# Performance work log

Measured on AMD Instinct MI355X. Metric: run time of the kernel, lower is better.

Reference implementation:

```python
import jax, jax.numpy as jnp
import numpy as np

B, S, E, D, H, L = 128, 50, 512, 1024, 16, 4
V, NU, NF, NR = 100000, 50000, 10000, 5
DK = D // H
FF = 4 * D


def _pe(S, D):
    # FranchisePositionalEncoding: two interleaved sin/cos halves (chrono + release*1.5)
    half = D // 2
    pos = jnp.arange(S, dtype=jnp.float32)[:, None]
    div = jnp.exp(jnp.arange(0, half, 2, dtype=jnp.float32) * (-np.log(10000.0) / half))
    def il(a):
        return jnp.stack([jnp.sin(a), jnp.cos(a)], axis=-1).reshape(S, half)
    return jnp.concatenate([il(pos * div), il(pos * div * 1.5)], axis=-1)  # [S, D]


def _ln(x, g, b):
    m = x.mean(-1, keepdims=True)
    v = ((x - m) ** 2).mean(-1, keepdims=True)
    return (x - m) * jax.lax.rsqrt(v + 1e-5) * g + b


def _gelu(x):
    return jax.nn.gelu(x, approximate=False)


def setup_inputs() -> dict:
    key = jax.random.key(0)
    ks = iter(jax.random.split(key, 64))
    def p(shape, s=0.02):
        return jax.random.normal(next(ks), shape, jnp.float32) * s
    inp = {
        'movie_table': p((V, E)), 'fran_table': p((NF, E)), 'entry_table': p((NR, E)),
        'proj_w': p((3 * E, D)), 'proj_b': jnp.zeros((D,), jnp.float32),
        'wq': p((L, D, D)), 'bq': jnp.zeros((L, D), jnp.float32),
        'wk': p((L, D, D)), 'bk': jnp.zeros((L, D), jnp.float32),
        'wv': p((L, D, D)), 'bv': jnp.zeros((L, D), jnp.float32),
        'wo': p((L, D, D)), 'bo': jnp.zeros((L, D), jnp.float32),
        'rel_table': p((L, NR, DK)),
        'aln_g': jnp.ones((L, D), jnp.float32), 'aln_b': jnp.zeros((L, D), jnp.float32),
        'f_w1': p((L, D, FF)), 'f_b1': jnp.zeros((L, FF), jnp.float32),
        'f_w2': p((L, FF, D)), 'f_b2': jnp.zeros((L, D), jnp.float32),
        'ln_g': jnp.ones((L, D), jnp.float32), 'ln_b': jnp.zeros((L, D), jnp.float32),
        'user_table': p((NU, D)),
        'mq_w': p((D, D)), 'mq_b': jnp.zeros((D,), jnp.float32),
        'mk_w': p((D, D)), 'mk_b': jnp.zeros((D,), jnp.float32),
        'mv_w': p((D, D)), 'mv_b': jnp.zeros((D,), jnp.float32),
        'mo_w': p((D, D)), 'mo_b': jnp.zeros((D,), jnp.float32),
        'c_w1': p((2 * D, D)), 'c_b1': jnp.zeros((D,), jnp.float32),
        'c_w2': p((D, 1)), 'c_b2': jnp.zeros((1,), jnp.float32),
        'n_w1': p((2 * D, D)), 'n_b1': jnp.zeros((D,), jnp.float32),
        'n_w2': p((D, V)), 'n_b2': jnp.zeros((V,), jnp.float32),
        'r_w1': p((3 * D, D)), 'r_b1': jnp.zeros((D,), jnp.float32),
        'r_w2': p((D, 1)), 'r_b2': jnp.zeros((1,), jnp.float32),
        'o_w1': p((D, D // 2)), 'o_b1': jnp.zeros((D // 2,), jnp.float32),
        'o_w2': p((D // 2, 2)), 'o_b2': jnp.zeros((2,), jnp.float32),
        'user_ids': jax.random.randint(next(ks), (B,), 0, NU),
        'movie_ids': jax.random.randint(next(ks), (B, S), 0, V),
        'franchise_ids': jax.random.randint(next(ks), (B, S), 0, NF),
        'entry_types': jax.random.randint(next(ks), (B, S), 0, NR),
        'relation_matrix': jax.random.randint(next(ks), (S, S), 0, NR),
    }
    return inp


def reference(movie_table, fran_table, entry_table, proj_w, proj_b,
              wq, bq, wk, bk, wv, bv, wo, bo, rel_table, aln_g, aln_b,
              f_w1, f_b1, f_w2, f_b2, ln_g, ln_b, user_table,
              mq_w, mq_b, mk_w, mk_b, mv_w, mv_b, mo_w, mo_b,
              c_w1, c_b1, c_w2, c_b2, n_w1, n_b1, n_w2, n_b2,
              r_w1, r_b1, r_w2, r_b2, o_w1, o_b1, o_w2, o_b2,
              user_ids, movie_ids, franchise_ids, entry_types, relation_matrix):
    b, s = movie_ids.shape
    d = proj_w.shape[1]
    nl, _, dk = rel_table.shape
    h = d // dk
    scale = 1.0 / np.sqrt(dk).astype(np.float32)

    # encoder input: concat(movie, franchise, entry) embeddings -> proj -> +PE
    x = jnp.concatenate([movie_table[movie_ids], fran_table[franchise_ids],
                         entry_table[entry_types]], axis=-1) @ proj_w + proj_b
    x = x + _pe(s, d)

    for l in range(nl):
        res = x
        q = (x @ wq[l] + bq[l]).reshape(b, s, h, dk).transpose(0, 2, 1, 3)  # [b,h,s,dk]
        k = (x @ wk[l] + bk[l]).reshape(b, s, h, dk).transpose(0, 2, 1, 3)
        v = (x @ wv[l] + bv[l]).reshape(b, s, h, dk).transpose(0, 2, 1, 3)
        scores = jnp.einsum('bhid,bhjd->bhij', q, k) * scale
        rel = rel_table[l][relation_matrix]  # [s,s,dk]
        scores = scores + 0.5 * jnp.einsum('bhid,ijd->bhij', q, rel)
        attn = jax.nn.softmax(scores, axis=-1)
        ctx = jnp.einsum('bhij,bhjd->bhid', attn, v).transpose(0, 2, 1, 3).reshape(b, s, d)
        x = _ln(ctx @ wo[l] + bo[l] + res, aln_g[l], aln_b[l])
        ff = _gelu(x @ f_w1[l] + f_b1[l]) @ f_w2[l] + f_b2[l]
        x = _ln(x + ff, ln_g[l], ln_b[l])

    # user preference cross-attention (nn.MultiheadAttention, q_len=1)
    user_emb = user_table[user_ids]  # [b,d]
    qh = (user_emb @ mq_w + mq_b).reshape(b, h, dk)
    kh = (x @ mk_w + mk_b).reshape(b, s, h, dk)
    vh = (x @ mv_w + mv_b).reshape(b, s, h, dk)
    a = jax.nn.softmax(jnp.einsum('bhd,bshd->bhs', qh, kh) * scale, axis=-1)
    user_pref = jnp.einsum('bhs,bshd->bhd', a, vh).reshape(b, d) @ mo_w + mo_b

    seq_repr = x.mean(axis=1)  # mask is None path
    ci = jnp.concatenate([user_pref, seq_repr], axis=-1)
    completion = jax.nn.sigmoid(_gelu(ci @ c_w1 + c_b1) @ c_w2 + c_b2)
    next_logits = _gelu(ci @ n_w1 + n_b1) @ n_w2 + n_b2
    ri = jnp.concatenate([user_emb, user_pref, seq_repr], axis=-1)
    rating = _gelu(ri @ r_w1 + r_b1) @ r_w2 + r_b2
    order = jax.nn.softmax(_gelu(user_pref @ o_w1 + o_b1) @ o_w2 + o_b2, axis=-1)
    return (x, completion, next_logits, rating, order, user_pref)
```

## Files before the change

### kernel.cpp

```cpp
#include <hip/hip_runtime.h>
#include <hip/hip_bf16.h>
#include <math.h>

#define B_   128
#define S_   50
#define BS_  (B_*S_)
#define E_   512
#define D_   1024
#define H_   16
#define DK_  64
#define L_   4
#define FF_  4096
#define V_   100000

typedef short bf8_t __attribute__((ext_vector_type(8)));
typedef float f32x4 __attribute__((ext_vector_type(4)));
typedef float f32x16 __attribute__((ext_vector_type(16)));
typedef unsigned short u16;

__device__ __forceinline__ float gelu_exact(float x) {
    return 0.5f * x * (1.0f + erff(x * 0.70710678118654752440f));
}
__device__ __forceinline__ u16 f2bf(float f) {
    unsigned int u = __float_as_uint(f);
    return (u16)((u + 0x7FFFu + ((u >> 16) & 1u)) >> 16);
}
__device__ __forceinline__ float bf2f(u16 u) {
    return __uint_as_float(((unsigned int)u) << 16);
}

__device__ __forceinline__ void gload16(const u16* g, u16* l) {
    auto* g1 = reinterpret_cast<const __attribute__((address_space(1))) unsigned int*>(
                   reinterpret_cast<uintptr_t>(g));
    auto* l3 = reinterpret_cast<__attribute__((address_space(3))) unsigned int*>(
                   reinterpret_cast<uintptr_t>(l));
    __builtin_amdgcn_global_load_lds(g1, l3, 16, 0, 0);
}

__device__ __forceinline__ void wtrans_body(
    const float* __restrict__ W, u16* __restrict__ Wt,
    int K, int N, int nb, int kb, int dstRowOff)
{
    __shared__ float t[32][33];
    int c = threadIdx.x & 31, r0 = threadIdx.x >> 5;
    #pragma unroll
    for (int rr = 0; rr < 32; rr += 8)
        t[rr + r0][c] = W[(size_t)(kb + rr + r0) * N + nb + c];
    __syncthreads();
    #pragma unroll
    for (int rr = 0; rr < 32; rr += 8)
        Wt[(size_t)(dstRowOff + nb + rr + r0) * K + kb + c] = f2bf(t[c][rr + r0]);
}

__global__ __launch_bounds__(256) void wtrans(
    const float* __restrict__ W, u16* __restrict__ Wt,
    int K, int N, long srcLS, long dstLS, int dstRowOff)
{
    int l = blockIdx.z;
    wtrans_body(W + (size_t)l * srcLS, Wt + (size_t)l * dstLS,
                K, N, blockIdx.x * 32, blockIdx.y * 32, dstRowOff);
}

__global__ __launch_bounds__(256) void wtrans_qkv(
    const float* __restrict__ wq, const float* __restrict__ wk, const float* __restrict__ wv,
    u16* __restrict__ dst)
{
    int z = blockIdx.z;
    int l = z & 3, which = z >> 2;
    const float* W = (which == 0 ? wq : which == 1 ? wk : wv) + (size_t)l * (D_ * D_);
    u16* Wt = dst + (size_t)l * (3 * D_ * D_) + (size_t)which * (D_ * D_);
    wtrans_body(W, Wt, D_, D_, blockIdx.x * 32, blockIdx.y * 32, 0);
}

struct WT8 { const float* s[8]; u16* d[8]; };
__global__ __launch_bounds__(256) void wtrans8(WT8 p)
{
    int z = blockIdx.z;
    wtrans_body(p.s[z], p.d[z], D_, D_, blockIdx.x * 32, blockIdx.y * 32, 0);
}

__global__ __launch_bounds__(256) void wtrans_ff(
    const float* __restrict__ w1, const float* __restrict__ w2,
    u16* __restrict__ d1, u16* __restrict__ d2)
{
    if (blockIdx.z == 0)
        wtrans_body(w1, d1, D_, FF_, blockIdx.x * 32, blockIdx.y * 32, 0);
    else
        wtrans_body(w2, d2, FF_, D_, blockIdx.y * 32, blockIdx.x * 32, 0);
}

__global__ __launch_bounds__(256) void embed_concat(
    const float* __restrict__ mt, const float* __restrict__ ft, const float* __restrict__ et,
    const int* __restrict__ mids, const int* __restrict__ fids, const int* __restrict__ eids,
    u16* __restrict__ xinb)
{
    int bs = blockIdx.x;
    int mid = mids[bs], fid = fids[bs], eid = eids[bs];
    const float* srcs[3] = { mt + (size_t)mid * E_, ft + (size_t)fid * E_, et + (size_t)eid * E_ };
    u16* dst = xinb + (size_t)bs * (3 * E_);
    for (int i = threadIdx.x; i < 384; i += 256) {
        int seg = i >> 7, off = i & 127;
        float4 v = reinterpret_cast<const float4*>(srcs[seg])[off];
        ushort4 b;
        b.x = f2bf(v.x); b.y = f2bf(v.y); b.z = f2bf(v.z); b.w = f2bf(v.w);
        reinterpret_cast<ushort4*>(dst + seg * E_)[off] = b;
    }
}

__global__ __launch_bounds__(256) void setup_misc(
    const float* __restrict__ bq, const float* __restrict__ bk, const float* __restrict__ bv,
    const float* __restrict__ cb1, const float* __restrict__ nb1,
    const float* __restrict__ mkb, const float* __restrict__ mvb,
    float* __restrict__ bqkv, float* __restrict__ bcn, float* __restrict__ bkv,
    float* __restrict__ pet)
{
    int bi = blockIdx.x, tid = threadIdx.x;
    if (bi < 4) {
        for (int c = tid; c < 3072; c += 256) {
            float v = (c < 1024) ? bq[bi * 1024 + c]
                    : (c < 2048) ? bk[bi * 1024 + c - 1024]
                                 : bv[bi * 1024 + c - 2048];
            bqkv[bi * 3072 + c] = v;
        }
    } else if (bi == 4) {
        for (int c = tid; c < 2048; c += 256)
            bcn[c] = (c < 1024) ? cb1[c] : nb1[c - 1024];
    } else if (bi == 5) {
        for (int c = tid; c < 2048; c += 256)
            bkv[c] = (c < 1024) ? mkb[c] : mvb[c - 1024];
    } else {
        int s = bi - 6;
        const float cc = -logf(10000.0f) / 512.0f;
        for (int d = tid; d < D_; d += 256) {
            int second = d >= 512;
            int c2 = second ? d - 512 : d;
            int i = c2 >> 1;
            float div = expf(cc * (float)(2 * i));
            float aa = (float)s * div * (second ? 1.5f : 1.0f);
            pet[s * D_ + d] = (c2 & 1) ? cosf(aa) : sinf(aa);
        }
    }
}

__global__ __launch_bounds__(256) void gemm128_w32(
    const u16* __restrict__ A, int lda, const u16* __restrict__ Wt,
    const float* __restrict__ bias,
    u16* __restrict__ Cb, int ldcb,
    int N, int K, int act)
{
    __shared__ u16 As[2 * 4096];
    __shared__ u16 Bs[2 * 4096];
    const int tid  = threadIdx.x;
    const int lane = tid & 63;
    const int wid  = tid >> 6;
    const int wr   = wid >> 1, wc = wid & 1;

    const int gx  = gridDim.x;
    const int nwg = gx * gridDim.y;
    int orig = blockIdx.y * gx + blockIdx.x;
    int qq = nwg >> 3, rr2 = nwg & 7, xcd = orig & 7, idx = orig >> 3;
    int wgid = (xcd < rr2) ? (xcd * (qq + 1) + idx)
                           : (rr2 * (qq + 1) + (xcd - rr2) * qq + idx);
    const int rowBase = (wgid / gx) * 128;
    const int colBase = (wgid % gx) * 128;

    const int sRowL  = lane >> 2;
    const int sChunk = lane & 3;
    const int gRow0  = (wid << 5) + sRowL;
    const int skey   = (gRow0 >> 1) & 3;
    const int gC     = (sChunk ^ skey) << 3;
    const u16* aS0 = A  + (size_t)(rowBase + gRow0) * lda + gC;
    const u16* aS1 = aS0 + (size_t)16 * lda;
    const u16* bS0 = Wt + (size_t)(colBase + gRow0) * K + gC;
    const u16* bS1 = bS0 + (size_t)16 * K;
    const int ldsW0 = (wid << 5) << 5;
    const int ldsW1 = ldsW0 + (16 << 5);

    const int l31 = lane & 31;
    const int hi5 = lane >> 5;
    const int key32 = (l31 >> 1) & 3;
    const int c0 = (0 | hi5) ^ key32;
    const int c1 = (2 | hi5) ^ key32;
    const int aB0 = (wr * 64 + l31) * 32;
    const int bB0 = (wc * 64 + l31) * 32;

    f32x16 acc[2][2] = {};
    const int nk = K >> 5;

    auto STAGE = [&](int kb, int buf) {
        u16* dA = As + buf * 4096;
        u16* dB = Bs + buf * 4096;
        gload16(aS0 + kb, dA + ldsW0);
        gload16(aS1 + kb, dA + ldsW1);
        gload16(bS0 + kb, dB + ldsW0);
        gload16(bS1 + kb, dB + ldsW1);
    };

    STAGE(0, 0);
    __builtin_amdgcn_sched_barrier(0);
    STAGE(32, 1);
    __builtin_amdgcn_sched_barrier(0);
    asm volatile("s_waitcnt vmcnt(4)\n\ts_barrier" ::: "memory");
    __builtin_amdgcn_sched_barrier(0);

    for (int t = 0; t < nk; ++t) {
        const int cur = t & 1;
        const u16* bA = As + cur * 4096;
        const u16* bB = Bs + cur * 4096;
        bf8_t aF[2][2], bF[2][2];
        #pragma unroll
        for (int mi = 0; mi < 2; ++mi) {
            aF[mi][0] = *reinterpret_cast<const bf8_t*>(&bA[aB0 + mi * 1024 + c0 * 8]);
            aF[mi][1] = *reinterpret_cast<const bf8_t*>(&bA[aB0 + mi * 1024 + c1 * 8]);
        }
        #pragma unroll
        for (int ni = 0; ni < 2; ++ni) {
            bF[ni][0] = *reinterpret_cast<const bf8_t*>(&bB[bB0 + ni * 1024 + c0 * 8]);
            bF[ni][1] = *reinterpret_cast<const bf8_t*>(&bB[bB0 + ni * 1024 + c1 * 8]);
        }
        #pragma unroll
        for (int mi = 0; mi < 2; ++mi)
            #pragma unroll
            for (int ni = 0; ni < 2; ++ni) {
                acc[mi][ni] = __builtin_amdgcn_mfma_f32_32x32x16_bf16(aF[mi][0], bF[ni][0], acc[mi][ni], 0, 0, 0);
                acc[mi][ni] = __builtin_amdgcn_mfma_f32_32x32x16_bf16(aF[mi][1], bF[ni][1], acc[mi][ni], 0, 0, 0);
            }
        if (t == nk - 1) break;
        __builtin_amdgcn_sched_barrier(0);
        asm volatile("s_waitcnt lgkmcnt(0)\n\ts_barrier" ::: "memory");
        __builtin_amdgcn_sched_barrier(0);
        if (t + 2 < nk) {
            STAGE((t + 2) << 5, cur);
            __builtin_amdgcn_sched_barrier(0);
            asm volatile("s_waitcnt vmcnt(4)\n\ts_barrier" ::: "memory");
        } else {
            asm volatile("s_waitcnt vmcnt(0)\n\ts_barrier" ::: "memory");
        }
        __builtin_amdgcn_sched_barrier(0);
    }

    #pragma unroll
    for (int mi = 0; mi < 2; ++mi) {
        int rt = rowBase + wr * 64 + mi * 32 + 4 * hi5;
        #pragma unroll
        for (int ni = 0; ni < 2; ++ni) {
            int ct = colBase + wc * 64 + ni * 32 + l31;
            float bv = bias ? bias[ct] : 0.0f;
            #pragma unroll
            for (int r = 0; r < 16; ++r) {
                int rr = rt + (r & 3) + 8 * (r >> 2);
                float v = acc[mi][ni][r] + bv;
                if (act == 1) v = gelu_exact(v);
                Cb[(size_t)rr * ldcb + ct] = f2bf(v);
            }
        }
    }
}

__global__ __launch_bounds__(256) void gemm_sk32(
    const u16* __restrict__ A, int lda, const u16* __restrict__ Wt, int ldb,
    u16* __restrict__ P0, u16* __restrict__ P1,
    int N, int Kh)
{
    __shared__ u16 As[2 * 4096];
    __shared__ u16 Bs[2 * 4096];
    const int tid  = threadIdx.x;
    const int lane = tid & 63;
    const int wid  = tid >> 6;
    const int wr   = wid >> 1, wc = wid & 1;

    const int gx  = gridDim.x;
    const int nwg = gx * gridDim.y;
    int orig = blockIdx.y * gx + blockIdx.x;
    int qq = nwg >> 3, rr2 = nwg & 7, xcd = orig & 7, idx = orig >> 3;
    int wgid = (xcd < rr2) ? (xcd * (qq + 1) + idx)
                           : (rr2 * (qq + 1) + (xcd - rr2) * qq + idx);
    const int rowBase = (wgid / gx) * 128;
    const int colBase = (wgid % gx) * 128;
    const int k0 = blockIdx.z * Kh;
    u16* P = blockIdx.z ? P1 : P0;

    const int sRowL  = lane >> 2;
    const int sChunk = lane & 3;
    const int gRow0  = (wid << 5) + sRowL;
    const int skey   = (gRow0 >> 1) & 3;
    const int gC     = (sChunk ^ skey) << 3;
    const u16* aS0 = A  + (size_t)(rowBase + gRow0) * lda + k0 + gC;
    const u16* aS1 = aS0 + (size_t)16 * lda;
    const u16* bS0 = Wt + (size_t)(colBase + gRow0) * ldb + k0 + gC;
    const u16* bS1 = bS0 + (size_t)16 * ldb;
    const int ldsW0 = (wid << 5) << 5;
    const int ldsW1 = ldsW0 + (16 << 5);

    const int l31 = lane & 31;
    const int hi5 = lane >> 5;
    const int key32 = (l31 >> 1) & 3;
    const int c0 = (0 | hi5) ^ key32;
    const int c1 = (2 | hi5) ^ key32;
    const int aB0 = (wr * 64 + l31) * 32;
    const int bB0 = (wc * 64 + l31) * 32;

    f32x16 acc[2][2] = {};
    const int nk = Kh >> 5;

    auto STAGE = [&](int kb, int buf) {
        u16* dA = As + buf * 4096;
        u16* dB = Bs + buf * 4096;
        gload16(aS0 + kb, dA + ldsW0);
        gload16(aS1 + kb, dA + ldsW1);
        gload16(bS0 + kb, dB + ldsW0);
        gload16(bS1 + kb, dB + ldsW1);
    };

    STAGE(0, 0);
    __builtin_amdgcn_sched_barrier(0);
    STAGE(32, 1);
    __builtin_amdgcn_sched_barrier(0);
    asm volatile("s_waitcnt vmcnt(4)\n\ts_barrier" ::: "memory");
    __builtin_amdgcn_sched_barrier(0);

    for (int t = 0; t < nk; ++t) {
        const int cur = t & 1;
        const u16* bA = As + cur * 4096;
        const u16* bB = Bs + cur * 4096;
        bf8_t aF[2][2], bF[2][2];
        #pragma unroll
        for (int mi = 0; mi < 2; ++mi) {
            aF[mi][0] = *reinterpret_cast<const bf8_t*>(&bA[aB0 + mi * 1024 + c0 * 8]);
            aF[mi][1] = *reinterpret_cast<const bf8_t*>(&bA[aB0 + mi * 1024 + c1 * 8]);
        }
        #pragma unroll
        for (int ni = 0; ni < 2; ++ni) {
            bF[ni][0] = *reinterpret_cast<const bf8_t*>(&bB[bB0 + ni * 1024 + c0 * 8]);
            bF[ni][1] = *reinterpret_cast<const bf8_t*>(&bB[bB0 + ni * 1024 + c1 * 8]);
        }
        #pragma unroll
        for (int mi = 0; mi < 2; ++mi)
            #pragma unroll
            for (int ni = 0; ni < 2; ++ni) {
                acc[mi][ni] = __builtin_amdgcn_mfma_f32_32x32x16_bf16(aF[mi][0], bF[ni][0], acc[mi][ni], 0, 0, 0);
                acc[mi][ni] = __builtin_amdgcn_mfma_f32_32x32x16_bf16(aF[mi][1], bF[ni][1], acc[mi][ni], 0, 0, 0);
            }
        if (t == nk - 1) break;
        __builtin_amdgcn_sched_barrier(0);
        asm volatile("s_waitcnt lgkmcnt(0)\n\ts_barrier" ::: "memory");
        __builtin_amdgcn_sched_barrier(0);
        if (t + 2 < nk) {
            STAGE((t + 2) << 5, cur);
            __builtin_amdgcn_sched_barrier(0);
            asm volatile("s_waitcnt vmcnt(4)\n\ts_barrier" ::: "memory");
        } else {
            asm volatile("s_waitcnt vmcnt(0)\n\ts_barrier" ::: "memory");
        }
        __builtin_amdgcn_sched_barrier(0);
    }

    #pragma unroll
    for (int mi = 0; mi < 2; ++mi) {
        int rt = rowBase + wr * 64 + mi * 32 + 4 * hi5;
        #pragma unroll
        for (int ni = 0; ni < 2; ++ni) {
            int ct = colBase + wc * 64 + ni * 32 + l31;
            #pragma unroll
            for (int r = 0; r < 16; ++r) {
                int rr = rt + (r & 3) + 8 * (r >> 2);
                P[(size_t)rr * N + ct] = f2bf(acc[mi][ni][r]);
            }
        }
    }
}

__global__ __launch_bounds__(256) void combine_bias_pe(
    const u16* __restrict__ p1, const u16* __restrict__ p2,
    const float* __restrict__ bias, const float* __restrict__ pe,
    u16* __restrict__ outb)
{
    int row = blockIdx.x, tid = threadIdx.x;
    int c0 = tid << 2;
    size_t base = (size_t)row * D_ + c0;
    ushort4 v1 = *reinterpret_cast<const ushort4*>(p1 + base);
    ushort4 v2 = *reinterpret_cast<const ushort4*>(p2 + base);
    float4 bv = *reinterpret_cast<const float4*>(bias + c0);
    float4 pv = *reinterpret_cast<const float4*>(pe + (size_t)(row % S_) * D_ + c0);
    ushort4 ob;
    ob.x = f2bf(bf2f(v1.x) + bf2f(v2.x) + bv.x + pv.x);
    ob.y = f2bf(bf2f(v1.y) + bf2f(v2.y) + bv.y + pv.y);
    ob.z = f2bf(bf2f(v1.z) + bf2f(v2.z) + bv.z + pv.z);
    ob.w = f2bf(bf2f(v1.w) + bf2f(v2.w) + bv.w + pv.w);
    *reinterpret_cast<ushort4*>(outb + base) = ob;
}

__global__ __launch_bounds__(256) void add_ln2(
    const u16* __restrict__ p1, const u16* __restrict__ p2,
    const float* __restrict__ bias, const u16* __restrict__ res,
    const float* __restrict__ g, const float* __restrict__ be,
    u16* __restrict__ outb, float* __restrict__ outf)
{
    int row = blockIdx.x, tid = threadIdx.x;
    int c0 = tid << 2;
    size_t base = (size_t)row * D_ + c0;
    ushort4 v1 = *reinterpret_cast<const ushort4*>(p1 + base);
    ushort4 v2 = *reinterpret_cast<const ushort4*>(p2 + base);
    float4 bv = *reinterpret_cast<const float4*>(bias + c0);
    ushort4 vr = *reinterpret_cast<const ushort4*>(res + base);
    float vals[4] = { bf2f(v1.x) + bf2f(v2.x) + bv.x + bf2f(vr.x),
                      bf2f(v1.y) + bf2f(v2.y) + bv.y + bf2f(vr.y),
                      bf2f(v1.z) + bf2f(v2.z) + bv.z + bf2f(vr.z),
                      bf2f(v1.w) + bf2f(v2.w) + bv.w + bf2f(vr.w) };
    float s = vals[0] + vals[1] + vals[2] + vals[3];
    __shared__ float red[8];
    #pragma unroll
    for (int off = 32; off; off >>= 1) s += __shfl_xor(s, off);
    int wave = tid >> 6, lane = tid & 63;
    if (lane == 0) red[wave] = s;
    __syncthreads();
    float mean = (red[0] + red[1] + red[2] + red[3]) * (1.0f / D_);
    float vv = 0.0f;
    #pragma unroll
    for (int t = 0; t < 4; ++t) {
        float d = vals[t] - mean;
        vv += d * d;
    }
    #pragma unroll
    for (int off = 32; off; off >>= 1) vv += __shfl_xor(vv, off);
    if (lane == 0) red[4 + wave] = vv;
    __syncthreads();
    float var = (red[4] + red[5] + red[6] + red[7]) * (1.0f / D_);
    float rstd = rsqrtf(var + 1e-5f);
    float4 gv  = *reinterpret_cast<const float4*>(g  + c0);
    float4 bev = *reinterpret_cast<const float4*>(be + c0);
    float o0 = (vals[0] - mean) * rstd * gv.x + bev.x;
    float o1 = (vals[1] - mean) * rstd * gv.y + bev.y;
    float o2 = (vals[2] - mean) * rstd * gv.z + bev.z;
    float o3 = (vals[3] - mean) * rstd * gv.w + bev.w;
    ushort4 ob;
    ob.x = f2bf(o0); ob.y = f2bf(o1); ob.z = f2bf(o2); ob.w = f2bf(o3);
    *reinterpret_cast<ushort4*>(outb + base) = ob;
    if (outf) {
        float4 of = { o0, o1, o2, o3 };
        *reinterpret_cast<float4*>(outf + base) = of;
    }
}

template<int BM>
__global__ __launch_bounds__(256) void gemm_bf16_t(
    const u16* __restrict__ A, int lda, const u16* __restrict__ Wt,
    const float* __restrict__ bias, float* __restrict__ Cf,
    u16* __restrict__ Cb, int ldcb, u16* __restrict__ Cb2, int ldcb2,
    int N, int K, int act)
{
    constexpr int MR   = BM / 32;
    constexpr int AL   = BM / 64;
    constexpr int ABUF = BM * 32;
    __shared__ u16 As[2 * ABUF];
    __shared__ u16 Bs[2 * 4096];
    const int tid  = threadIdx.x;
    const int lane = tid & 63;
    const int wid  = tid >> 6;
    const int wr   = wid >> 1, wc = wid & 1;

    const int rowBase = blockIdx.y * BM;
    const int colBase = blockIdx.x * 128;

    const int fr = lane & 15;
    const int hi = lane >> 4;

    const int sRowL  = lane >> 2;
    const int sChunk = lane & 3;
    const int aRow0 = wid * (BM / 4) + sRowL;
    const int aKey  = (aRow0 >> 1) & 3;
    const u16* aS0 = A + (size_t)(rowBase + aRow0) * lda + ((sChunk ^ aKey) << 3);
    const u16* aS1 = aS0 + (size_t)16 * lda;
    const int ldsA0 = (wid * (BM / 4)) * 32;
    const int ldsA1 = ldsA0 + 512;
    const int bRow0 = wid * 32 + sRowL;
    const int bKey  = (bRow0 >> 1) & 3;
    const u16* bS0 = Wt + (size_t)(colBase + bRow0) * K + ((sChunk ^ bKey) << 3);
    const u16* bS1 = bS0 + (size_t)16 * K;
    const int ldsB0 = (wid * 32) * 32;
    const int ldsB1 = ldsB0 + 512;

    const int swz = ((hi ^ ((fr >> 1) & 3)) << 3);
    const int aRd = (wr * (BM / 2) + fr) * 32 + swz;
    const int bRd = (wc * 64 + fr) * 32 + swz;

    f32x4 acc[MR][4] = {};
    const int nk = K >> 5;

    auto STAGE = [&](int kb, int buf) {
        u16* dA = As + buf * ABUF;
        u16* dB = Bs + buf * 4096;
        gload16(aS0 + kb, dA + ldsA0);
        if constexpr (AL == 2) gload16(aS1 + kb, dA + ldsA1);
        gload16(bS0 + kb, dB + ldsB0);
        gload16(bS1 + kb, dB + ldsB1);
    };

    STAGE(0, 0);
    __builtin_amdgcn_sched_barrier(0);
    STAGE(32, 1);
    __builtin_amdgcn_sched_barrier(0);
    if constexpr (BM == 128) asm volatile("s_waitcnt vmcnt(4)\n\ts_barrier" ::: "memory");
    else                     asm volatile("s_waitcnt vmcnt(3)\n\ts_barrier" ::: "memory");
    __builtin_amdgcn_sched_barrier(0);

    for (int t = 0; t < nk; ++t) {
        const int cur = t & 1;
        const u16* bA = As + cur * ABUF;
        const u16* bB = Bs + cur * 4096;
        bf8_t af[MR], bf[4];
        #pragma unroll
        for (int m = 0; m < MR; ++m)
            af[m] = *reinterpret_cast<const bf8_t*>(&bA[aRd + m * 512]);
        #pragma unroll
        for (int n = 0; n < 4; ++n)
            bf[n] = *reinterpret_cast<const bf8_t*>(&bB[bRd + n * 512]);
        #pragma unroll
        for (int m = 0; m < MR; ++m)
            #pragma unroll
            for (int n = 0; n < 4; ++n)
                acc[m][n] = __builtin_amdgcn_mfma_f32_16x16x32_bf16(af[m], bf[n], acc[m][n], 0, 0, 0);
        if (t == nk - 1) break;
        __builtin_amdgcn_sched_barrier(0);
        asm volatile("s_waitcnt lgkmcnt(0)\n\ts_barrier" ::: "memory");
        __builtin_amdgcn_sched_barrier(0);
        if (t + 2 < nk) {
            STAGE((t + 2) << 5, cur);
            __builtin_amdgcn_sched_barrier(0);
            if constexpr (BM == 128) asm volatile("s_waitcnt vmcnt(4)\n\ts_barrier" ::: "memory");
            else                     asm volatile("s_waitcnt vmcnt(3)\n\ts_barrier" ::: "memory");
        } else {
            asm volatile("s_waitcnt vmcnt(0)\n\ts_barrier" ::: "memory");
        }
        __builtin_amdgcn_sched_barrier(0);
    }

    const int orow = hi << 2;
    #pragma unroll
    for (int m = 0; m < MR; ++m) {
        int r0 = rowBase + wr * (BM / 2) + m * 16 + orow;
        #pragma unroll
        for (int n = 0; n < 4; ++n) {
            int c = colBase + wc * 64 + n * 16 + fr;
            float bv = bias ? bias[c] : 0.0f;
            #pragma unroll
            for (int r = 0; r < 4; ++r) {
                float v = acc[m][n][r] + bv;
                if (act == 1) v = gelu_exact(v);
                if (Cf)  Cf [(size_t)(r0 + r) * N + c] = v;
                if (Cb)  Cb [(size_t)(r0 + r) * ldcb  + c] = f2bf(v);
                if (Cb2) Cb2[(size_t)(r0 + r) * ldcb2 + c] = f2bf(v);
            }
        }
    }
}

__global__ __launch_bounds__(256) void gemm_logits(
    const float* __restrict__ A, int lda, const float* __restrict__ W,
    const float* __restrict__ bias, float* __restrict__ C, int N, int K)
{
    __shared__ u16 As[2][128][40];
    __shared__ u16 Bs[2][128][40];
    const int tid  = threadIdx.x;
    const int lane = tid & 63;
    const int wid  = tid >> 6;
    const int wr   = wid >> 1, wc = wid & 1;
    const int colBase = blockIdx.x * 128;

    const int a_r = tid >> 1;
    const int a_h = (tid & 1) << 4;
    const int b_c = tid & 127;
    const int b_h = (tid >> 7) << 4;

    const int fr = lane & 15;
    const int fk = (lane >> 4) << 3;

    f32x4 acc[4][4] = {};
    const int nvalid = N - colBase;
    const bool valid = b_c < nvalid;
    const int nk = K >> 5;

    float4 aR[4];
    float  bR[16];

    auto LD = [&](int kb) {
        const float* Ap = A + (size_t)a_r * lda + kb + a_h;
        #pragma unroll
        for (int q = 0; q < 4; ++q)
            aR[q] = *reinterpret_cast<const float4*>(Ap + q * 4);
        const float* Wp = W + (size_t)(kb + b_h) * N + colBase + b_c;
        #pragma unroll
        for (int kk = 0; kk < 16; ++kk)
            bR[kk] = valid ? Wp[(size_t)kk * N] : 0.0f;
    };
    auto ST = [&](int buf) {
        #pragma unroll
        for (int q = 0; q < 4; ++q) {
            ushort4 bb;
            bb.x = f2bf(aR[q].x); bb.y = f2bf(aR[q].y);
            bb.z = f2bf(aR[q].z); bb.w = f2bf(aR[q].w);
            *reinterpret_cast<ushort4*>(&As[buf][a_r][a_h + q * 4]) = bb;
        }
        u16 tmp[16];
        #pragma unroll
        for (int kk = 0; kk < 16; ++kk) tmp[kk] = f2bf(bR[kk]);
        *reinterpret_cast<bf8_t*>(&Bs[buf][b_c][b_h])     = *reinterpret_cast<const bf8_t*>(tmp);
        *reinterpret_cast<bf8_t*>(&Bs[buf][b_c][b_h + 8]) = *reinterpret_cast<const bf8_t*>(tmp + 8);
    };

    LD(0); ST(0);
    __syncthreads();

    for (int t = 0; t < nk; ++t) {
        if (t + 1 < nk) LD((t + 1) << 5);
        const int cur = t & 1;
        bf8_t af[4], bfv[4];
        #pragma unroll
        for (int m = 0; m < 4; ++m)
            af[m] = *reinterpret_cast<const bf8_t*>(&As[cur][wr * 64 + m * 16 + fr][fk]);
        #pragma unroll
        for (int n = 0; n < 4; ++n)
            bfv[n] = *reinterpret_cast<const bf8_t*>(&Bs[cur][wc * 64 + n * 16 + fr][fk]);
        #pragma unroll
        for (int m = 0; m < 4; ++m)
            #pragma unroll
            for (int n = 0; n < 4; ++n)
                acc[m][n] = __builtin_amdgcn_mfma_f32_16x16x32_bf16(af[m], bfv[n], acc[m][n], 0, 0, 0);
        if (t + 1 < nk) ST(cur ^ 1);
        __syncthreads();
    }

    const int orow = (lane >> 4) << 2;
    #pragma unroll
    for (int m = 0; m < 4; ++m) {
        int r0 = wr * 64 + m * 16 + orow;
        #pragma unroll
        for (int n = 0; n < 4; ++n) {
            int c = colBase + wc * 64 + n * 16 + fr;
            if (c < N) {
                float bv = bias ? bias[c] : 0.0f;
                #pragma unroll
                for (int r = 0; r < 4; ++r)
                    C[(size_t)(r0 + r) * N + c] = acc[m][n][r] + bv;
            }
        }
    }
}

__global__ __launch_bounds__(256) void attn_kernel(
    const u16* __restrict__ qkv, const float* __restrict__ rt, const int* __restrict__ rm,
    u16* __restrict__ ctxb)
{
    int bh = blockIdx.x;
    int b = bh >> 4, h = bh & 15;
    __shared__ float qs[S_][DK_ + 1], ks[S_][DK_ + 1], vs[S_][DK_ + 1];
    __shared__ float rts[5][DK_];
    __shared__ float Rs[S_][8];
    int tid = threadIdx.x;
    int wave = tid >> 6, lane = tid & 63;

    for (int idx = tid; idx < S_ * DK_; idx += 256) {
        int s = idx >> 6, d = idx & 63;
        size_t g = ((size_t)(b * S_ + s)) * (3 * D_) + h * DK_ + d;
        qs[s][d] = bf2f(qkv[g]);
        ks[s][d] = bf2f(qkv[g + D_]);
        vs[s][d] = bf2f(qkv[g + 2 * D_]);
    }
    for (int i = tid; i < 5 * DK_; i += 256)
        rts[i >> 6][i & 63] = rt[i];
    __syncthreads();

    for (int t = tid; t < S_ * 5; t += 256) {
        int i = t / 5, r = t - 5 * i;
        float a = 0.0f;
        #pragma unroll 8
        for (int d = 0; d < DK_; ++d) a += qs[i][d] * rts[r][d];
        Rs[i][r] = a;
    }
    __syncthreads();

    const float scale = 0.125f;
    for (int i = wave; i < S_; i += 4) {
        float sc = -INFINITY;
        if (lane < S_) {
            float acc = 0.0f;
            #pragma unroll 8
            for (int d = 0; d < DK_; ++d) acc += qs[i][d] * ks[lane][d];
            sc = acc * scale + 0.5f * Rs[i][rm[i * S_ + lane]];
        }
        float m = sc;
        #pragma unroll
        for (int off = 32; off; off >>= 1) m = fmaxf(m, __shfl_xor(m, off));
        float e = (lane < S_) ? expf(sc - m) : 0.0f;
        float sum = e;
        #pragma unroll
        for (int off = 32; off; off >>= 1) sum += __shfl_xor(sum, off);
        float aval = e / sum;

        float acc = 0.0f;
        for (int j = 0; j < S_; ++j) {
            float aj = __shfl(aval, j);
            acc += aj * vs[j][lane];
        }
        ctxb[((size_t)(b * S_ + i)) * D_ + h * DK_ + lane] = f2bf(acc);
    }
}

__global__ __launch_bounds__(256) void gather_user(
    const float* __restrict__ ut, const int* __restrict__ ids,
    u16* __restrict__ o1, int ld1, u16* __restrict__ o2, int ld2)
{
    int b = blockIdx.x;
    int uid = ids[b];
    for (int d = threadIdx.x; d < D_; d += 256) {
        u16 v = f2bf(ut[(size_t)uid * D_ + d]);
        o1[(size_t)b * ld1 + d] = v;
        o2[(size_t)b * ld2 + d] = v;
    }
}

__global__ __launch_bounds__(64) void cross_attn(
    const u16* __restrict__ qh, const u16* __restrict__ kv, u16* __restrict__ up)
{
    int bh = blockIdx.x;
    int b = bh >> 4, h = bh & 15;
    int lane = threadIdx.x;
    __shared__ float qv[DK_];
    qv[lane] = bf2f(qh[(size_t)b * D_ + h * DK_ + lane]);
    __syncthreads();
    float sc = -INFINITY;
    if (lane < S_) {
        float acc = 0.0f;
        const u16* krow = kv + ((size_t)(b * S_ + lane)) * 2048 + h * DK_;
        #pragma unroll 8
        for (int d = 0; d < DK_; ++d) acc += qv[d] * bf2f(krow[d]);
        sc = acc * 0.125f;
    }
    float m = sc;
    #pragma unroll
    for (int off = 32; off; off >>= 1) m = fmaxf(m, __shfl_xor(m, off));
    float e = (lane < S_) ? expf(sc - m) : 0.0f;
    float sum = e;
    #pragma unroll
    for (int off = 32; off; off >>= 1) sum += __shfl_xor(sum, off);
    float aval = e / sum;
    float acc = 0.0f;
    for (int j = 0; j < S_; ++j) {
        float aj = __shfl(aval, j);
        acc += aj * bf2f(kv[((size_t)(b * S_ + j)) * 2048 + 1024 + h * DK_ + lane]);
    }
    up[(size_t)b * D_ + h * DK_ + lane] = f2bf(acc);
}

__global__ __launch_bounds__(256) void seq_mean(
    const float* __restrict__ x,
    u16* __restrict__ o1, int ld1, u16* __restrict__ o2, int ld2)
{
    int b = blockIdx.x;
    for (int d = threadIdx.x; d < D_; d += 256) {
        float s = 0.0f;
        for (int si = 0; si < S_; ++si)
            s += x[((size_t)(b * S_ + si)) * D_ + d];
        u16 v = f2bf(s * (1.0f / S_));
        o1[(size_t)b * ld1 + d] = v;
        o2[(size_t)b * ld2 + d] = v;
    }
}

__global__ __launch_bounds__(256) void heads_final(
    const float* __restrict__ h1cn, const float* __restrict__ h1r, const float* __restrict__ ho,
    const float* __restrict__ c_w2, const float* __restrict__ c_b2,
    const float* __restrict__ r_w2, const float* __restrict__ r_b2,
    const float* __restrict__ o_w2, const float* __restrict__ o_b2,
    float* __restrict__ comp, float* __restrict__ rating, float* __restrict__ order)
{
    int b = blockIdx.x;
    int lane = threadIdx.x & 63, wv = threadIdx.x >> 6;
    if (wv == 0) {
        float s = 0.0f;
        for (int d = lane; d < D_; d += 64) s += h1cn[(size_t)b * 2048 + d] * c_w2[d];
        #pragma unroll
        for (int off = 32; off; off >>= 1) s += __shfl_xor(s, off);
        if (lane == 0) comp[b] = 1.0f / (1.0f + expf(-(s + c_b2[0])));
    } else if (wv == 1) {
        float s = 0.0f;
        for (int d = lane; d < D_; d += 64) s += h1r[(size_t)b * D_ + d] * r_w2[d];
        #pragma unroll
        for (int off = 32; off; off >>= 1) s += __shfl_xor(s, off);
        if (lane == 0) rating[b] = s + r_b2[0];
    } else if (wv == 2) {
        float s0 = 0.0f, s1 = 0.0f;
        for (int d = lane; d < 512; d += 64) {
            float hv = ho[(size_t)b * 512 + d];
            s0 += hv * o_w2[d * 2];
            s1 += hv * o_w2[d * 2 + 1];
        }
        #pragma unroll
        for (int off = 32; off; off >>= 1) { s0 += __shfl_xor(s0, off); s1 += __shfl_xor(s1, off); }
        if (lane == 0) {
            float a = s0 + o_b2[0], c = s1 + o_b2[1];
            float m = fmaxf(a, c);
            float ea = expf(a - m), ec = expf(c - m);
            float s = ea + ec;
            order[b * 2] = ea / s;
            order[b * 2 + 1] = ec / s;
        }
    }
}

extern "C" void kernel_launch(void* const* d_in, const int* in_sizes, int n_in,
                              void* d_out, int out_size, void* d_ws, size_t ws_size,
                              hipStream_t stream) {
    const float* movie_table = (const float*)d_in[0];
    const float* fran_table  = (const float*)d_in[1];
    const float* entry_table = (const float*)d_in[2];
    const float* proj_w      = (const float*)d_in[3];
    const float* proj_b      = (const float*)d_in[4];
    const float* wq          = (const float*)d_in[5];
    const float* bq          = (const float*)d_in[6];
    const float* wk          = (const float*)d_in[7];
    const float* bk          = (const float*)d_in[8];
    const float* wv          = (const float*)d_in[9];
    const float* bv          = (const float*)d_in[10];
    const float* wo          = (const float*)d_in[11];
    const float* bo          = (const float*)d_in[12];
    const float* rel_table   = (const float*)d_in[13];
    const float* aln_g       = (const float*)d_in[14];
    const float* aln_b       = (const float*)d_in[15];
    const float* f_w1        = (const float*)d_in[16];
    const float* f_b1        = (const float*)d_in[17];
    const float* f_w2        = (const float*)d_in[18];
    const float* f_b2        = (const float*)d_in[19];
    const float* ln_g        = (const float*)d_in[20];
    const float* ln_b        = (const float*)d_in[21];
    const float* user_table  = (const float*)d_in[22];
    const float* mq_w        = (const float*)d_in[23];
    const float* mq_b        = (const float*)d_in[24];
    const float* mk_w        = (const float*)d_in[25];
    const float* mk_b        = (const float*)d_in[26];
    const float* mv_w        = (const float*)d_in[27];
    const float* mv_b        = (const float*)d_in[28];
    const float* mo_w        = (const float*)d_in[29];
    const float* mo_b        = (const float*)d_in[30];
    const float* c_w1        = (const float*)d_in[31];
    const float* c_b1        = (const float*)d_in[32];
    const float* c_w2        = (const float*)d_in[33];
    const float* c_b2        = (const float*)d_in[34];
    const float* n_w1        = (const float*)d_in[35];
    const float* n_b1        = (const float*)d_in[36];
    const float* n_w2        = (const float*)d_in[37];
    const float* n_b2        = (const float*)d_in[38];
    const float* r_w1        = (const float*)d_in[39];
    const float* r_b1        = (const float*)d_in[40];
    const float* r_w2        = (const float*)d_in[41];
    const float* r_b2        = (const float*)d_in[42];
    const float* o_w1        = (const float*)d_in[43];
    const float* o_b1        = (const float*)d_in[44];
    const float* o_w2        = (const float*)d_in[45];
    const float* o_b2        = (const float*)d_in[46];
    const int* user_ids      = (const int*)d_in[47];
    const int* movie_ids     = (const int*)d_in[48];
    const int* franchise_ids = (const int*)d_in[49];
    const int* entry_types   = (const int*)d_in[50];
    const int* relation_mat  = (const int*)d_in[51];

    u16* up16 = (u16*)d_ws;
    u16* proj_wt = up16;
    u16* wqkv_t  = proj_wt + (size_t)1024 * 1536;
    u16* wo_t    = wqkv_t  + (size_t)4 * 3072 * 1024;
    u16* fw1_buf = wo_t    + (size_t)4 * 1024 * 1024;
    u16* fw2_buf = fw1_buf + (size_t)4096 * 1024;
    u16* mq_t    = fw2_buf + (size_t)1024 * 4096;
    u16* mk_t    = mq_t    + (size_t)1024 * 1024;
    u16* mv_t    = mk_t    + (size_t)1024 * 1024;
    u16* mo_t    = mv_t    + (size_t)1024 * 1024;
    u16* cn_w1t  = mo_t    + (size_t)1024 * 1024;
    u16* r_w1t   = cn_w1t  + (size_t)2048 * 2048;
    u16* o_w1t   = r_w1t   + (size_t)1024 * 3072;
    u16* ffb     = o_w1t   + (size_t)512 * 1024;
    u16* xinb    = ffb;
    u16* xb      = ffb     + (size_t)BS_ * FF_;
    u16* xb2     = xb      + (size_t)BS_ * D_;
    u16* qkvb    = xb2     + (size_t)BS_ * D_;
    u16* kvb     = qkvb    + (size_t)BS_ * 3 * D_;
    u16* ctxb    = kvb;
    u16* ueb     = kvb     + (size_t)BS_ * 2 * D_;
    u16* upb_pre = ueb     + (size_t)B_ * D_;
    u16* cib     = upb_pre + (size_t)B_ * D_;
    u16* rib     = cib     + (size_t)B_ * 2 * D_;
    float* fp    = (float*)(rib + (size_t)B_ * 3 * D_);
    float* bqkv  = fp;
    float* bcn   = bqkv + 4 * 3072;
    float* bkv   = bcn  + 2048;
    float* pet   = bkv  + 2048;
    float* h1cn  = pet  + 50 * 1024;
    float* h1r   = h1cn + (size_t)B_ * 2048;
    float* ho    = h1r  + (size_t)B_ * D_;

    u16* pQK = qkvb;
    u16* pKV = kvb;
    u16* pFF = ffb;

    float* xout    = (float*)d_out;
    float* comp    = xout + (size_t)BS_ * D_;
    float* logits  = comp + B_;
    float* rating  = logits + (size_t)B_ * V_;
    float* order   = rating + B_;
    float* upref   = order + 2 * B_;

    dim3 blk(256);

    wtrans<<<dim3(32, 48, 1), blk, 0, stream>>>(proj_w, proj_wt, 1536, 1024, 0, 0, 0);
    wtrans_qkv<<<dim3(32, 32, 12), blk, 0, stream>>>(wq, wk, wv, wqkv_t);
    WT8 w8;
    w8.s[0] = wo;                 w8.d[0] = wo_t;
    w8.s[1] = wo + 1048576;       w8.d[1] = wo_t + 1048576;
    w8.s[2] = wo + 2097152;       w8.d[2] = wo_t + 2097152;
    w8.s[3] = wo + 3145728;       w8.d[3] = wo_t + 3145728;
    w8.s[4] = mq_w;               w8.d[4] = mq_t;
    w8.s[5] = mk_w;               w8.d[5] = mk_t;
    w8.s[6] = mv_w;               w8.d[6] = mv_t;
    w8.s[7] = mo_w;               w8.d[7] = mo_t;
    wtrans8<<<dim3(32, 32, 8), blk, 0, stream>>>(w8);
    wtrans<<<dim3(32, 64, 1), blk, 0, stream>>>(c_w1, cn_w1t, 2048, 1024, 0, 0, 0);
    wtrans<<<dim3(32, 64, 1), blk, 0, stream>>>(n_w1, cn_w1t, 2048, 1024, 0, 0, 1024);
    wtrans<<<dim3(32, 96, 1), blk, 0, stream>>>(r_w1, r_w1t, 3072, 1024, 0, 0, 0);
    wtrans<<<dim3(16, 32, 1), blk, 0, stream>>>(o_w1, o_w1t, 1024, 512, 0, 0, 0);
    setup_misc<<<dim3(56), blk, 0, stream>>>(bq, bk, bv, c_b1, n_b1, mk_b, mv_b,
                                             bqkv, bcn, bkv, pet);

    embed_concat<<<BS_, blk, 0, stream>>>(movie_table, fran_table, entry_table,
                                          movie_ids, franchise_ids, entry_types, xinb);
    gemm_sk32<<<dim3(8, 50, 2), blk, 0, stream>>>(xinb, 1536, proj_wt, 1536,
                                                  pQK, pKV, D_, 768);
    combine_bias_pe<<<BS_, blk, 0, stream>>>(pQK, pKV, proj_b, pet, xb);

    for (int l = 0; l < L_; ++l) {
        gemm128_w32<<<dim3(24, 50), blk, 0, stream>>>(xb, 1024,
                wqkv_t + (size_t)l * 3145728, bqkv + l * 3072,
                qkvb, 3072, 3 * D_, D_, 0);
        attn_kernel<<<B_ * H_, blk, 0, stream>>>(qkvb, rel_table + (size_t)l * 5 * DK_,
                                                 relation_mat, ctxb);
        gemm_sk32<<<dim3(8, 50, 2), blk, 0, stream>>>(ctxb, 1024,
                wo_t + (size_t)l * 1048576, 1024, pQK, pFF, D_, 512);
        add_ln2<<<BS_, blk, 0, stream>>>(pQK, pFF, bo + l * D_, xb,
                                         aln_g + l * D_, aln_b + l * D_, xb2, nullptr);
        wtrans_ff<<<dim3(128, 32, 2), blk, 0, stream>>>(f_w1 + (size_t)l * D_ * FF_,
                                                        f_w2 + (size_t)l * FF_ * D_,
                                                        fw1_buf, fw2_buf);
        gemm128_w32<<<dim3(32, 50), blk, 0, stream>>>(xb2, 1024, fw1_buf, f_b1 + l * FF_,
                ffb, 4096, FF_, D_, 1);
        gemm_sk32<<<dim3(8, 50, 2), blk, 0, stream>>>(ffb, 4096, fw2_buf, 4096,
                                                      pQK, pKV, D_, 2048);
        add_ln2<<<BS_, blk, 0, stream>>>(pQK, pKV, f_b2 + l * D_, xb2,
                                         ln_g + l * D_, ln_b + l * D_, xb,
                                         (l == L_ - 1) ? xout : nullptr);
    }

    gather_user<<<B_, blk, 0, stream>>>(user_table, user_ids, ueb, 1024, rib, 3072);
    gemm_bf16_t<64><<<dim3(8, 2), blk, 0, stream>>>(ueb, 1024, mq_t, mq_b,
            nullptr, qkvb, 1024, nullptr, 0, D_, D_, 0);
    gemm128_w32<<<dim3(16, 50), blk, 0, stream>>>(xb, 1024, mk_t, bkv,
            kvb, 2048, 2 * D_, D_, 0);
    cross_attn<<<B_ * H_, dim3(64), 0, stream>>>(qkvb, kvb, upb_pre);
    gemm_bf16_t<64><<<dim3(8, 2), blk, 0, stream>>>(upb_pre, 1024, mo_t, mo_b,
            upref, cib, 2048, rib + 1024, 3072, D_, D_, 0);

    seq_mean<<<B_, blk, 0, stream>>>(xout, cib + 1024, 2048, rib + 2048, 3072);

    gemm_bf16_t<64><<<dim3(16, 2), blk, 0, stream>>>(cib, 2048, cn_w1t, bcn,
            h1cn, nullptr, 0, nullptr, 0, 2048, 2048, 1);
    gemm_bf16_t<64><<<dim3(8, 2), blk, 0, stream>>>(rib, 3072, r_w1t, r_b1,
            h1r, nullptr, 0, nullptr, 0, D_, 3072, 1);
    gemm_bf16_t<64><<<dim3(4, 2), blk, 0, stream>>>(cib, 2048, o_w1t, o_b1,
            ho, nullptr, 0, nullptr, 0, 512, D_, 1);
    gemm_logits<<<dim3(782, 1), blk, 0, stream>>>(h1cn + 1024, 2048, n_w2, n_b2,
                                                  logits, V_, D_);
    heads_final<<<B_, blk, 0, stream>>>(h1cn, h1r, ho, c_w2, c_b2, r_w2, r_b2,
                                        o_w2, o_b2, comp, rating, order);
}
```

Measured before the change: 2.130 ms.

## Use triple-buffered LDS ring in GEMM kernels with one barrier per k-step

Both the bias/GELU GEMM and the split-K GEMM go from a two-slot LDS buffer to a three-slot ring. The next-but-one tile's global-to-LDS load now issues right after the current fragments are read and before the MFMAs, and only one waitcnt+barrier remains per iteration instead of two. This is meant to cut barrier stalls and overlap global loads with MFMA work, at the cost of 1.5x LDS per workgroup, which may reduce occupancy.

```diff
diff --git a/kernel.cpp b/kernel.cpp
--- a/kernel.cpp
+++ b/kernel.cpp
@@ -148,8 +148,8 @@
     u16* __restrict__ Cb, int ldcb,
     int N, int K, int act)
 {
-    __shared__ u16 As[2 * 4096];
-    __shared__ u16 Bs[2 * 4096];
+    __shared__ u16 As[3 * 4096];
+    __shared__ u16 Bs[3 * 4096];
     const int tid  = threadIdx.x;
     const int lane = tid & 63;
     const int wid  = tid >> 6;
@@ -200,11 +200,12 @@
     __builtin_amdgcn_sched_barrier(0);
     STAGE(32, 1);
     __builtin_amdgcn_sched_barrier(0);
-    asm volatile("s_waitcnt vmcnt(4)\n\ts_barrier" ::: "memory");
-    __builtin_amdgcn_sched_barrier(0);
-
+
+    int cur = 0;
     for (int t = 0; t < nk; ++t) {
-        const int cur = t & 1;
+        if (t < nk - 1) asm volatile("s_waitcnt vmcnt(4) lgkmcnt(0)\n\ts_barrier" ::: "memory");
+        else            asm volatile("s_waitcnt vmcnt(0) lgkmcnt(0)\n\ts_barrier" ::: "memory");
+        __builtin_amdgcn_sched_barrier(0);
         const u16* bA = As + cur * 4096;
         const u16* bB = Bs + cur * 4096;
         bf8_t aF[2][2], bF[2][2];
@@ -218,6 +219,11 @@
             bF[ni][0] = *reinterpret_cast<const bf8_t*>(&bB[bB0 + ni * 1024 + c0 * 8]);
             bF[ni][1] = *reinterpret_cast<const bf8_t*>(&bB[bB0 + ni * 1024 + c1 * 8]);
         }
+        if (t + 2 < nk) {
+            int nb = cur + 2; if (nb >= 3) nb -= 3;
+            STAGE((t + 2) << 5, nb);
+        }
+        __builtin_amdgcn_sched_barrier(0);
         #pragma unroll
         for (int mi = 0; mi < 2; ++mi)
             #pragma unroll
@@ -225,18 +231,7 @@
                 acc[mi][ni] = __builtin_amdgcn_mfma_f32_32x32x16_bf16(aF[mi][0], bF[ni][0], acc[mi][ni], 0, 0, 0);
                 acc[mi][ni] = __builtin_amdgcn_mfma_f32_32x32x16_bf16(aF[mi][1], bF[ni][1], acc[mi][ni], 0, 0, 0);
             }
-        if (t == nk - 1) break;
-        __builtin_amdgcn_sched_barrier(0);
-        asm volatile("s_waitcnt lgkmcnt(0)\n\ts_barrier" ::: "memory");
-        __builtin_amdgcn_sched_barrier(0);
-        if (t + 2 < nk) {
-            STAGE((t + 2) << 5, cur);
-            __builtin_amdgcn_sched_barrier(0);
-            asm volatile("s_waitcnt vmcnt(4)\n\ts_barrier" ::: "memory");
-        } else {
-            asm volatile("s_waitcnt vmcnt(0)\n\ts_barrier" ::: "memory");
-        }
-        __builtin_amdgcn_sched_barrier(0);
+        cur = (cur == 2) ? 0 : cur + 1;
     }
 
     #pragma unroll
@@ -262,8 +257,8 @@
     u16* __restrict__ P0, u16* __restrict__ P1,
     int N, int Kh)
 {
-    __shared__ u16 As[2 * 4096];
-    __shared__ u16 Bs[2 * 4096];
+    __shared__ u16 As[3 * 4096];
+    __shared__ u16 Bs[3 * 4096];
     const int tid  = threadIdx.x;
     const int lane = tid & 63;
     const int wid  = tid >> 6;
@@ -316,11 +311,12 @@
     __builtin_amdgcn_sched_barrier(0);
     STAGE(32, 1);
     __builtin_amdgcn_sched_barrier(0);
-    asm volatile("s_waitcnt vmcnt(4)\n\ts_barrier" ::: "memory");
-    __builtin_amdgcn_sched_barrier(0);
-
+
+    int cur = 0;
     for (int t = 0; t < nk; ++t) {
-        const int cur = t & 1;
+        if (t < nk - 1) asm volatile("s_waitcnt vmcnt(4) lgkmcnt(0)\n\ts_barrier" ::: "memory");
+        else            asm volatile("s_waitcnt vmcnt(0) lgkmcnt(0)\n\ts_barrier" ::: "memory");
+        __builtin_amdgcn_sched_barrier(0);
         const u16* bA = As + cur * 4096;
         const u16* bB = Bs + cur * 4096;
         bf8_t aF[2][2], bF[2][2];
@@ -334,6 +330,11 @@
             bF[ni][0] = *reinterpret_cast<const bf8_t*>(&bB[bB0 + ni * 1024 + c0 * 8]);
             bF[ni][1] = *reinterpret_cast<const bf8_t*>(&bB[bB0 + ni * 1024 + c1 * 8]);
         }
+        if (t + 2 < nk) {
+            int nb = cur + 2; if (nb >= 3) nb -= 3;
+            STAGE((t + 2) << 5, nb);
+        }
+        __builtin_amdgcn_sched_barrier(0);
         #pragma unroll
         for (int mi = 0; mi < 2; ++mi)
             #pragma unroll
@@ -341,18 +342,7 @@
                 acc[mi][ni] = __builtin_amdgcn_mfma_f32_32x32x16_bf16(aF[mi][0], bF[ni][0], acc[mi][ni], 0, 0, 0);
                 acc[mi][ni] = __builtin_amdgcn_mfma_f32_32x32x16_bf16(aF[mi][1], bF[ni][1], acc[mi][ni], 0, 0, 0);
             }
-        if (t == nk - 1) break;
-        __builtin_amdgcn_sched_barrier(0);
-        asm volatile("s_waitcnt lgkmcnt(0)\n\ts_barrier" ::: "memory");
-        __builtin_amdgcn_sched_barrier(0);
-        if (t + 2 < nk) {
-            STAGE((t + 2) << 5, cur);
-            __builtin_amdgcn_sched_barrier(0);
-            asm volatile("s_waitcnt vmcnt(4)\n\ts_barrier" ::: "memory");
-        } else {
-            asm volatile("s_waitcnt vmcnt(0)\n\ts_barrier" ::: "memory");
-        }
-        __builtin_amdgcn_sched_barrier(0);
+        cur = (cur == 2) ? 0 : cur + 1;
     }
 
     #pragma unroll
```

New measurement: 2.109 ms, median of 2. No clear change (-1.0%).
